# Optimization experiments

Hardware: AMD Instinct MI355X
Metric: run time of the kernel (lower is better)

Reference implementation:

```python
import jax, jax.numpy as jnp
import numpy as np

B, T, D, H = 2, 2048, 1024, 16
STD = 0.02

def setup_inputs() -> dict:
    key = jax.random.key(0)
    ks = jax.random.split(key, 5)
    x = jax.random.normal(ks[0], (B, T, D), dtype=jnp.float32)
    Wq = jax.random.normal(ks[1], (D, D), dtype=jnp.float32) * STD
    Wk = jax.random.normal(ks[2], (D, D), dtype=jnp.float32) * STD
    Wv = jax.random.normal(ks[3], (D, D), dtype=jnp.float32) * STD
    Wo = jax.random.normal(ks[4], (D, D), dtype=jnp.float32) * STD
    z = jnp.zeros((D,), dtype=jnp.float32)
    return {"x": x, "Wq": Wq, "bq": z, "Wk": Wk, "bk": z, "Wv": Wv, "bv": z, "Wo": Wo, "bo": z}

def _split(t, h):
    b, s, dm = t.shape
    return t.reshape(b, s, h, dm // h).transpose(0, 2, 1, 3)  # (B,h,T,d)

def reference(x, Wq, bq, Wk, bk, Wv, bv, Wo, bo):
    h = H
    # linear projections (nn.Linear: y = x @ W^T + b)
    q = _split(x @ Wq.T + bq, h)
    k = _split(x @ Wk.T + bk, h)
    v = _split(x @ Wv.T + bv, h)
    d_k = k.shape[-1]
    # scaled dot-product similarities (B,h,T,T)
    sim = jnp.einsum("bhqd,bhkd->bhqk", q, k) / jnp.sqrt(jnp.float32(d_k))
    # causal mask: upper triangle (excluding diag) filled with -inf
    Tq = sim.shape[-1]
    causal = jnp.tril(jnp.ones((Tq, Tq), dtype=bool))
    sim = jnp.where(causal, sim, -jnp.inf)
    attn = jax.nn.softmax(sim, axis=-1)
    ctx = jnp.einsum("bhqk,bhkd->bhqd", attn, v)  # (B,h,T,d)
    ctx = ctx.transpose(0, 2, 1, 3).reshape(x.shape[0], x.shape[1], -1)  # (B,T,D)
    return ctx @ Wo.T + bo
```

## Files before the change

kernel.cpp:

```cpp
#include <hip/hip_runtime.h>
#include <hip/hip_bf16.h>


typedef __attribute__((ext_vector_type(8))) short bf16x8;
typedef __attribute__((ext_vector_type(4))) float f32x4;
typedef __attribute__((ext_vector_type(4))) short s16x4;

#define QSCALE 0.18033688011f

__device__ __forceinline__ int sniff_f32(const void* p) {
    const unsigned short* u = (const unsigned short*)p;
    int c = 0;
    for (int i = 0; i < 256; ++i) {
        int e = (u[i] >> 7) & 0xFF;
        c += (e >= 0x90) ? 1 : 0;
    }
    return c > 8;
}

__device__ __forceinline__ void async_copy16(const void* g, void* l) {
    __builtin_amdgcn_global_load_lds(
        (const __attribute__((address_space(1))) void*)g,
        (__attribute__((address_space(3))) void*)l, 16, 0, 0);
}

struct Cvt { const void* src; __hip_bfloat16* dst; int n; };
struct CvtPack { Cvt a[9]; };

__global__ __launch_bounds__(256) void cvt_bf16(CvtPack pk) {
    const Cvt c = pk.a[blockIdx.y];
    const int f32 = sniff_f32(c.src);
    const int stride = gridDim.x * 256 * 8;
    for (int idx = (blockIdx.x * 256 + threadIdx.x) * 8; idx < c.n; idx += stride) {
        if (f32) {
            const float* s = (const float*)c.src + idx;
            f32x4 a0 = *(const f32x4*)s;
            f32x4 a1 = *(const f32x4*)(s + 4);
            union { __hip_bfloat16 h[8]; bf16x8 v; } u;
#pragma unroll
            for (int e = 0; e < 4; e++) u.h[e]     = (__hip_bfloat16)a0[e];
#pragma unroll
            for (int e = 0; e < 4; e++) u.h[4 + e] = (__hip_bfloat16)a1[e];
            *(bf16x8*)&c.dst[idx] = u.v;
        } else {
            *(bf16x8*)&c.dst[idx] = *(const bf16x8*)((const __hip_bfloat16*)c.src + idx);
        }
    }
}

template <int MODE>
__device__ __forceinline__ void gemm_async_body(
    const __hip_bfloat16* __restrict__ A, const __hip_bfloat16* __restrict__ W,
    const __hip_bfloat16* __restrict__ bias, void* __restrict__ C,
    int M, int N, int K, int bm, int bn, float outscale,
    __hip_bfloat16* sA, __hip_bfloat16* sB)
{
    const int tid  = threadIdx.x;
    const int wave = tid >> 6;
    const int lane = tid & 63;
    const int quad = lane >> 4;
    const int l15  = lane & 15;
    const int wr   = wave >> 1;
    const int wc   = wave & 1;

    const int srow = wave * 16 + (lane >> 2);
    const int scol = (lane & 3) * 8;
    const __hip_bfloat16* gA0 = A + (size_t)(bm + srow) * K + scol;
    const __hip_bfloat16* gB0 = W + (size_t)(bn + srow) * K + scol;
    __hip_bfloat16* sA0 = sA + wave * 512;
    __hip_bfloat16* sB0 = sB + wave * 512;

    f32x4 acc[4][4];
#pragma unroll
    for (int i = 0; i < 4; i++)
#pragma unroll
        for (int j = 0; j < 4; j++) acc[i][j] = (f32x4)0.0f;

    for (int k0 = 0; k0 < K; k0 += 32) {
        __syncthreads();
#pragma unroll
        for (int r = 0; r < 2; r++) {
            async_copy16(gA0 + (size_t)r * 64 * K + k0, sA0 + r * 2048);
            async_copy16(gB0 + (size_t)r * 64 * K + k0, sB0 + r * 2048);
        }
        __syncthreads();

        bf16x8 af[4], bf[4];
#pragma unroll
        for (int i = 0; i < 4; i++)
            af[i] = *(const bf16x8*)&sA[(wr * 64 + i * 16 + l15) * 32 + quad * 8];
#pragma unroll
        for (int j = 0; j < 4; j++)
            bf[j] = *(const bf16x8*)&sB[(wc * 64 + j * 16 + l15) * 32 + quad * 8];
#pragma unroll
        for (int i = 0; i < 4; i++)
#pragma unroll
            for (int j = 0; j < 4; j++)
                acc[i][j] = __builtin_amdgcn_mfma_f32_16x16x32_bf16(af[i], bf[j], acc[i][j], 0, 0, 0);
    }

    float bv[4];
#pragma unroll
    for (int j = 0; j < 4; j++)
        bv[j] = (float)bias[bn + wc * 64 + j * 16 + l15];

    if (MODE == 2) {
        __hip_bfloat16* VTo = (__hip_bfloat16*)C;
#pragma unroll
        for (int i = 0; i < 4; i++) {
            int tglob = bm + wr * 64 + i * 16 + quad * 4;
            int bb = tglob >> 11, tt = tglob & 2047;
#pragma unroll
            for (int j = 0; j < 4; j++) {
                int d = bn + wc * 64 + j * 16 + l15;
                int hh = d >> 6, dh = d & 63;
                union { __hip_bfloat16 e[4]; s16x4 v; } u;
#pragma unroll
                for (int r = 0; r < 4; r++)
                    u.e[r] = (__hip_bfloat16)(acc[i][j][r] + bv[j]);
                *(s16x4*)&VTo[(((size_t)bb * 16 + hh) * 64 + dh) * 2048 + tt] = u.v;
            }
        }
    } else {
#pragma unroll
        for (int i = 0; i < 4; i++) {
#pragma unroll
            for (int j = 0; j < 4; j++) {
                int col = bn + wc * 64 + j * 16 + l15;
#pragma unroll
                for (int r = 0; r < 4; r++) {
                    int row = bm + wr * 64 + i * 16 + quad * 4 + r;
                    float v = (acc[i][j][r] + bv[j]) * outscale;
                    if (MODE == 1) ((float*)C)[(size_t)row * N + col] = v;
                    else ((__hip_bfloat16*)C)[(size_t)row * N + col] = (__hip_bfloat16)v;
                }
            }
        }
    }
}

__global__ __launch_bounds__(256, 2) void qkv_gemm(
    const __hip_bfloat16* __restrict__ x,
    const __hip_bfloat16* __restrict__ Wq, const __hip_bfloat16* __restrict__ bq, __hip_bfloat16* __restrict__ Q,
    const __hip_bfloat16* __restrict__ Wk, const __hip_bfloat16* __restrict__ bk, __hip_bfloat16* __restrict__ Kb,
    const __hip_bfloat16* __restrict__ Wv, const __hip_bfloat16* __restrict__ bv, __hip_bfloat16* __restrict__ VT,
    int M, int N, int K)
{
    __shared__ __hip_bfloat16 sA[128 * 32];
    __shared__ __hip_bfloat16 sB[128 * 32];
    if (blockIdx.z == 0)
        gemm_async_body<0>(x, Wq, bq, Q, M, N, K, blockIdx.x * 128, blockIdx.y * 128, QSCALE, sA, sB);
    else if (blockIdx.z == 1)
        gemm_async_body<0>(x, Wk, bk, Kb, M, N, K, blockIdx.x * 128, blockIdx.y * 128, 1.0f, sA, sB);
    else
        gemm_async_body<2>(x, Wv, bv, VT, M, N, K, blockIdx.x * 128, blockIdx.y * 128, 1.0f, sA, sB);
}

template <bool OF32>
__device__ __forceinline__ void gemm64_body(
    const __hip_bfloat16* __restrict__ A, const __hip_bfloat16* __restrict__ W,
    const __hip_bfloat16* __restrict__ bias, void* __restrict__ C,
    int M, int N, int K, int bm, int bn,
    __hip_bfloat16* sA, __hip_bfloat16* sB)
{
    const int tid  = threadIdx.x;
    const int wave = tid >> 6;
    const int lane = tid & 63;
    const int quad = lane >> 4;
    const int l15  = lane & 15;

    const int srow = wave * 16 + (lane >> 2);
    const int scol = (lane & 3) * 8;
    const __hip_bfloat16* gA0 = A + (size_t)(bm + srow) * K + scol;
    const __hip_bfloat16* gB0 = W + (size_t)(bn + srow) * K + scol;
    __hip_bfloat16* sA0 = sA + wave * 512;
    __hip_bfloat16* sB0 = sB + wave * 512;

    f32x4 acc[4][2];
#pragma unroll
    for (int i = 0; i < 4; i++)
#pragma unroll
        for (int j = 0; j < 2; j++) acc[i][j] = (f32x4)0.0f;

    for (int k0 = 0; k0 < K; k0 += 32) {
        __syncthreads();
        async_copy16(gA0 + k0, sA0);
#pragma unroll
        for (int r = 0; r < 2; r++)
            async_copy16(gB0 + (size_t)r * 64 * K + k0, sB0 + r * 2048);
        __syncthreads();

        bf16x8 af[4], bf[2];
#pragma unroll
        for (int i = 0; i < 4; i++)
            af[i] = *(const bf16x8*)&sA[(i * 16 + l15) * 32 + quad * 8];
#pragma unroll
        for (int j = 0; j < 2; j++)
            bf[j] = *(const bf16x8*)&sB[(wave * 32 + j * 16 + l15) * 32 + quad * 8];
#pragma unroll
        for (int i = 0; i < 4; i++)
#pragma unroll
            for (int j = 0; j < 2; j++)
                acc[i][j] = __builtin_amdgcn_mfma_f32_16x16x32_bf16(af[i], bf[j], acc[i][j], 0, 0, 0);
    }

    float bv[2];
#pragma unroll
    for (int j = 0; j < 2; j++)
        bv[j] = (float)bias[bn + wave * 32 + j * 16 + l15];
#pragma unroll
    for (int i = 0; i < 4; i++) {
#pragma unroll
        for (int j = 0; j < 2; j++) {
            int col = bn + wave * 32 + j * 16 + l15;
#pragma unroll
            for (int r = 0; r < 4; r++) {
                int row = bm + i * 16 + quad * 4 + r;
                float v = acc[i][j][r] + bv[j];
                if (OF32) ((float*)C)[(size_t)row * N + col] = v;
                else      ((__hip_bfloat16*)C)[(size_t)row * N + col] = (__hip_bfloat16)v;
            }
        }
    }
}

__global__ __launch_bounds__(256, 2) void out_gemm(
    const __hip_bfloat16* __restrict__ A, const __hip_bfloat16* __restrict__ W,
    const __hip_bfloat16* __restrict__ bias, const void* __restrict__ origW,
    void* __restrict__ C, int M, int N, int K)
{
    __shared__ __hip_bfloat16 sA[64 * 32];
    __shared__ __hip_bfloat16 sB[128 * 32];
    __shared__ int f32flag;
    if (threadIdx.x == 0) f32flag = sniff_f32(origW);
    __syncthreads();
    if (f32flag)
        gemm64_body<true>(A, W, bias, C, M, N, K, blockIdx.x * 64, blockIdx.y * 128, sA, sB);
    else
        gemm64_body<false>(A, W, bias, C, M, N, K, blockIdx.x * 64, blockIdx.y * 128, sA, sB);
}

#define PAD 68

__global__ __launch_bounds__(256, 2) void attn_causal(
    const __hip_bfloat16* __restrict__ Q,
    const __hip_bfloat16* __restrict__ K,
    const __hip_bfloat16* __restrict__ VT,
    __hip_bfloat16* __restrict__ O,
    int T, int D, int H)
{
    __shared__ __hip_bfloat16 sK[2][64 * PAD];
    __shared__ __hip_bfloat16 sVT[2][64 * PAD];
    __shared__ __hip_bfloat16 sPA[4][32 * PAD];

    const int tid  = threadIdx.x;
    const int wave = tid >> 6;
    const int lane = tid & 63;
    const int quad = lane >> 4;
    const int l15  = lane & 15;

    const int NT = T >> 7;
    const int qt = blockIdx.z ? (NT - 1 - (int)blockIdx.x) : (int)blockIdx.x;
    const int h  = blockIdx.y;
    const int b  = blockIdx.z;
    const size_t headoff = (size_t)b * T * D + (size_t)h * 64;
    const size_t vtoff   = ((size_t)b * H + h) * 64 * (size_t)T;

    const int nkt = 2 * qt + 2;
    const int myrowmax = qt * 128 + wave * 32 + 31;

    bf16x8 qfrag[2][2];
#pragma unroll
    for (int g = 0; g < 2; g++)
#pragma unroll
        for (int kk = 0; kk < 2; kk++)
            qfrag[g][kk] = *(const bf16x8*)&Q[headoff +
                (size_t)(qt * 128 + wave * 32 + g * 16 + l15) * D + kk * 32 + quad * 8];

    f32x4 acc_o[2][4];
#pragma unroll
    for (int g = 0; g < 2; g++)
#pragma unroll
        for (int j = 0; j < 4; j++) acc_o[g][j] = (f32x4)0.0f;
    float lacc[2] = {0.f, 0.f};

    const int srow = tid >> 3;
    const int sc8  = (tid & 7) * 8;

    bf16x8 pk[2], pv[2];
#pragma unroll
    for (int u = 0; u < 2; u++) {
        int row = srow + u * 32;
        pk[u] = *(const bf16x8*)&K[headoff + (size_t)row * D + sc8];
        pv[u] = *(const bf16x8*)&VT[vtoff + (size_t)row * T + sc8];
    }
#pragma unroll
    for (int u = 0; u < 2; u++) {
        int row = srow + u * 32;
        *(bf16x8*)&sK[0][row * PAD + sc8]  = pk[u];
        *(bf16x8*)&sVT[0][row * PAD + sc8] = pv[u];
    }
    if (nkt > 1) {
#pragma unroll
        for (int u = 0; u < 2; u++) {
            int row = srow + u * 32;
            pk[u] = *(const bf16x8*)&K[headoff + (size_t)(64 + row) * D + sc8];
            pv[u] = *(const bf16x8*)&VT[vtoff + (size_t)row * T + 64 + sc8];
        }
    }
    __syncthreads();

    for (int kt = 0; kt < nkt; ++kt) {
        const int cur = kt & 1;

        if (kt + 1 < nkt) {
#pragma unroll
            for (int u = 0; u < 2; u++) {
                int row = srow + u * 32;
                *(bf16x8*)&sK[1 - cur][row * PAD + sc8]  = pk[u];
                *(bf16x8*)&sVT[1 - cur][row * PAD + sc8] = pv[u];
            }
            if (kt + 2 < nkt) {
#pragma unroll
                for (int u = 0; u < 2; u++) {
                    int row = srow + u * 32;
                    pk[u] = *(const bf16x8*)&K[headoff + (size_t)((kt + 2) * 64 + row) * D + sc8];
                    pv[u] = *(const bf16x8*)&VT[vtoff + (size_t)row * T + (kt + 2) * 64 + sc8];
                }
            }
        }

        if (kt * 64 <= myrowmax) {
            bf16x8 kfrag[2][4], vfrag[2][4];
#pragma unroll
            for (int kk = 0; kk < 2; kk++)
#pragma unroll
                for (int j = 0; j < 4; j++) {
                    kfrag[kk][j] = *(const bf16x8*)&sK[cur][(j * 16 + l15) * PAD + kk * 32 + quad * 8];
                    vfrag[kk][j] = *(const bf16x8*)&sVT[cur][(j * 16 + l15) * PAD + kk * 32 + quad * 8];
                }

#pragma unroll
            for (int g = 0; g < 2; g++) {
                const int qbase = qt * 128 + wave * 32 + g * 16;
                f32x4 st[4];
#pragma unroll
                for (int j = 0; j < 4; j++) st[j] = (f32x4)0.0f;
#pragma unroll
                for (int kk = 0; kk < 2; kk++)
#pragma unroll
                    for (int j = 0; j < 4; j++)
                        st[j] = __builtin_amdgcn_mfma_f32_16x16x32_bf16(
                            kfrag[kk][j], qfrag[g][kk], st[j], 0, 0, 0);

                if (kt * 64 + 63 > qbase) {
                    const int q = qbase + l15;
#pragma unroll
                    for (int j = 0; j < 4; j++) {
                        int keyb = kt * 64 + j * 16 + quad * 4;
#pragma unroll
                        for (int r = 0; r < 4; r++)
                            if (keyb + r > q) st[j][r] = -1e30f;
                    }
                }

#pragma unroll
                for (int j = 0; j < 4; j++) {
                    union { __hip_bfloat16 e[4]; s16x4 v; } u;
#pragma unroll
                    for (int r = 0; r < 4; r++) {
                        float p = exp2f(st[j][r]);
                        lacc[g] += p;
                        u.e[r] = (__hip_bfloat16)p;
                    }
                    *(s16x4*)&sPA[wave][(g * 16 + l15) * PAD + j * 16 + quad * 4] = u.v;
                }
            }
#pragma unroll
            for (int g = 0; g < 2; g++)
#pragma unroll
                for (int kk = 0; kk < 2; kk++) {
                    bf16x8 a = *(const bf16x8*)&sPA[wave][(g * 16 + l15) * PAD + kk * 32 + quad * 8];
#pragma unroll
                    for (int j = 0; j < 4; j++)
                        acc_o[g][j] = __builtin_amdgcn_mfma_f32_16x16x32_bf16(
                            a, vfrag[kk][j], acc_o[g][j], 0, 0, 0);
                }
        }

        __syncthreads();
    }

#pragma unroll
    for (int g = 0; g < 2; g++) {
        lacc[g] += __shfl_xor(lacc[g], 16, 64);
        lacc[g] += __shfl_xor(lacc[g], 32, 64);
    }

#pragma unroll
    for (int g = 0; g < 2; g++)
#pragma unroll
        for (int r = 0; r < 4; r++) {
            float linv = 1.0f / __shfl(lacc[g], quad * 4 + r, 64);
            int row = qt * 128 + wave * 32 + g * 16 + quad * 4 + r;
#pragma unroll
            for (int j = 0; j < 4; j++) {
                int col = j * 16 + l15;
                O[headoff + (size_t)row * D + col] = (__hip_bfloat16)(acc_o[g][j][r] * linv);
            }
        }
}

extern "C" void kernel_launch(void* const* d_in, const int* in_sizes, int n_in,
                              void* d_out, int out_size, void* d_ws, size_t ws_size,
                              hipStream_t stream) {
    const int Bb = 2, T = 2048, D = 1024, H = 16;
    const int M = Bb * T;

    __hip_bfloat16* w = (__hip_bfloat16*)d_ws;
    __hip_bfloat16* Q   = w;
    __hip_bfloat16* Kb  = Q   + (size_t)M * D;
    __hip_bfloat16* VT  = Kb  + (size_t)M * D;
    __hip_bfloat16* ctx = VT  + (size_t)M * D;
    __hip_bfloat16* xb  = ctx + (size_t)M * D;
    __hip_bfloat16* Wqb = xb  + (size_t)M * D;
    __hip_bfloat16* Wkb = Wqb + (size_t)D * D;
    __hip_bfloat16* Wvb = Wkb + (size_t)D * D;
    __hip_bfloat16* Wob = Wvb + (size_t)D * D;
    __hip_bfloat16* bqb = Wob + (size_t)D * D;
    __hip_bfloat16* bkb = bqb + D;
    __hip_bfloat16* bvb = bkb + D;
    __hip_bfloat16* bob = bvb + D;

    CvtPack pk;
    pk.a[0] = { d_in[0], xb,  M * D };
    pk.a[1] = { d_in[1], Wqb, D * D };
    pk.a[2] = { d_in[2], bqb, D };
    pk.a[3] = { d_in[3], Wkb, D * D };
    pk.a[4] = { d_in[4], bkb, D };
    pk.a[5] = { d_in[5], Wvb, D * D };
    pk.a[6] = { d_in[6], bvb, D };
    pk.a[7] = { d_in[7], Wob, D * D };
    pk.a[8] = { d_in[8], bob, D };

    cvt_bf16<<<dim3(512, 9), 256, 0, stream>>>(pk);
    qkv_gemm<<<dim3(M / 128, D / 128, 3), 256, 0, stream>>>(
        xb, Wqb, bqb, Q, Wkb, bkb, Kb, Wvb, bvb, VT, M, D, D);
    attn_causal<<<dim3(T / 128, H, Bb), 256, 0, stream>>>(Q, Kb, VT, ctx, T, D, H);
    out_gemm<<<dim3(M / 64, D / 128), 256, 0, stream>>>(
        ctx, Wob, bob, d_in[7], d_out, M, D, D);
}
```

Measured before the change: 214.8 us.

## Split attention work across 8 waves of 16 query rows each

The causal attention kernel now runs 512 threads per block, so each of 8 waves owns 16 query rows instead of 4 waves owning 32. Each thread stages one K/V row per tile instead of two, which cuts per-thread registers. The change also adds s_setprio around the MFMA sections. It aims to raise occupancy and latency hiding. In exchange, each wave re-reads the K/V fragments from LDS for half as much work, and block barriers now synchronise more waves.

```diff
diff --git a/kernel.cpp b/kernel.cpp
--- a/kernel.cpp
+++ b/kernel.cpp
@@ -242,7 +242,7 @@
 
 #define PAD 68
 
-__global__ __launch_bounds__(256, 2) void attn_causal(
+__global__ __launch_bounds__(512, 4) void attn_causal(
     const __hip_bfloat16* __restrict__ Q,
     const __hip_bfloat16* __restrict__ K,
     const __hip_bfloat16* __restrict__ VT,
@@ -251,7 +251,7 @@
 {
     __shared__ __hip_bfloat16 sK[2][64 * PAD];
     __shared__ __hip_bfloat16 sVT[2][64 * PAD];
-    __shared__ __hip_bfloat16 sPA[4][32 * PAD];
+    __shared__ __hip_bfloat16 sPA[8][16 * PAD];
 
     const int tid  = threadIdx.x;
     const int wave = tid >> 6;
@@ -267,46 +267,31 @@
     const size_t vtoff   = ((size_t)b * H + h) * 64 * (size_t)T;
 
     const int nkt = 2 * qt + 2;
-    const int myrowmax = qt * 128 + wave * 32 + 31;
-
-    bf16x8 qfrag[2][2];
-#pragma unroll
-    for (int g = 0; g < 2; g++)
-#pragma unroll
-        for (int kk = 0; kk < 2; kk++)
-            qfrag[g][kk] = *(const bf16x8*)&Q[headoff +
-                (size_t)(qt * 128 + wave * 32 + g * 16 + l15) * D + kk * 32 + quad * 8];
-
-    f32x4 acc_o[2][4];
-#pragma unroll
-    for (int g = 0; g < 2; g++)
-#pragma unroll
-        for (int j = 0; j < 4; j++) acc_o[g][j] = (f32x4)0.0f;
-    float lacc[2] = {0.f, 0.f};
+    const int qbase    = qt * 128 + wave * 16;
+    const int myrowmax = qbase + 15;
+
+    bf16x8 qfrag[2];
+#pragma unroll
+    for (int kk = 0; kk < 2; kk++)
+        qfrag[kk] = *(const bf16x8*)&Q[headoff +
+            (size_t)(qbase + l15) * D + kk * 32 + quad * 8];
+
+    f32x4 acc_o[4];
+#pragma unroll
+    for (int j = 0; j < 4; j++) acc_o[j] = (f32x4)0.0f;
+    float lacc = 0.f;
 
     const int srow = tid >> 3;
     const int sc8  = (tid & 7) * 8;
 
-    bf16x8 pk[2], pv[2];
-#pragma unroll
-    for (int u = 0; u < 2; u++) {
-        int row = srow + u * 32;
-        pk[u] = *(const bf16x8*)&K[headoff + (size_t)row * D + sc8];
-        pv[u] = *(const bf16x8*)&VT[vtoff + (size_t)row * T + sc8];
-    }
-#pragma unroll
-    for (int u = 0; u < 2; u++) {
-        int row = srow + u * 32;
-        *(bf16x8*)&sK[0][row * PAD + sc8]  = pk[u];
-        *(bf16x8*)&sVT[0][row * PAD + sc8] = pv[u];
-    }
+    bf16x8 pk, pv;
+    pk = *(const bf16x8*)&K[headoff + (size_t)srow * D + sc8];
+    pv = *(const bf16x8*)&VT[vtoff + (size_t)srow * T + sc8];
+    *(bf16x8*)&sK[0][srow * PAD + sc8]  = pk;
+    *(bf16x8*)&sVT[0][srow * PAD + sc8] = pv;
     if (nkt > 1) {
-#pragma unroll
-        for (int u = 0; u < 2; u++) {
-            int row = srow + u * 32;
-            pk[u] = *(const bf16x8*)&K[headoff + (size_t)(64 + row) * D + sc8];
-            pv[u] = *(const bf16x8*)&VT[vtoff + (size_t)row * T + 64 + sc8];
-        }
+        pk = *(const bf16x8*)&K[headoff + (size_t)(64 + srow) * D + sc8];
+        pv = *(const bf16x8*)&VT[vtoff + (size_t)srow * T + 64 + sc8];
     }
     __syncthreads();
 
@@ -314,19 +299,11 @@
         const int cur = kt & 1;
 
         if (kt + 1 < nkt) {
-#pragma unroll
-            for (int u = 0; u < 2; u++) {
-                int row = srow + u * 32;
-                *(bf16x8*)&sK[1 - cur][row * PAD + sc8]  = pk[u];
-                *(bf16x8*)&sVT[1 - cur][row * PAD + sc8] = pv[u];
-            }
+            *(bf16x8*)&sK[1 - cur][srow * PAD + sc8]  = pk;
+            *(bf16x8*)&sVT[1 - cur][srow * PAD + sc8] = pv;
             if (kt + 2 < nkt) {
-#pragma unroll
-                for (int u = 0; u < 2; u++) {
-                    int row = srow + u * 32;
-                    pk[u] = *(const bf16x8*)&K[headoff + (size_t)((kt + 2) * 64 + row) * D + sc8];
-                    pv[u] = *(const bf16x8*)&VT[vtoff + (size_t)row * T + (kt + 2) * 64 + sc8];
-                }
+                pk = *(const bf16x8*)&K[headoff + (size_t)((kt + 2) * 64 + srow) * D + sc8];
+                pv = *(const bf16x8*)&VT[vtoff + (size_t)srow * T + (kt + 2) * 64 + sc8];
             }
         }
 
@@ -340,75 +317,68 @@
                     vfrag[kk][j] = *(const bf16x8*)&sVT[cur][(j * 16 + l15) * PAD + kk * 32 + quad * 8];
                 }
 
-#pragma unroll
-            for (int g = 0; g < 2; g++) {
-                const int qbase = qt * 128 + wave * 32 + g * 16;
-                f32x4 st[4];
-#pragma unroll
-                for (int j = 0; j < 4; j++) st[j] = (f32x4)0.0f;
-#pragma unroll
-                for (int kk = 0; kk < 2; kk++)
-#pragma unroll
-                    for (int j = 0; j < 4; j++)
-                        st[j] = __builtin_amdgcn_mfma_f32_16x16x32_bf16(
-                            kfrag[kk][j], qfrag[g][kk], st[j], 0, 0, 0);
-
-                if (kt * 64 + 63 > qbase) {
-                    const int q = qbase + l15;
-#pragma unroll
-                    for (int j = 0; j < 4; j++) {
-                        int keyb = kt * 64 + j * 16 + quad * 4;
-#pragma unroll
-                        for (int r = 0; r < 4; r++)
-                            if (keyb + r > q) st[j][r] = -1e30f;
-                    }
+            f32x4 st[4];
+#pragma unroll
+            for (int j = 0; j < 4; j++) st[j] = (f32x4)0.0f;
+            __builtin_amdgcn_s_setprio(1);
+#pragma unroll
+            for (int kk = 0; kk < 2; kk++)
+#pragma unroll
+                for (int j = 0; j < 4; j++)
+                    st[j] = __builtin_amdgcn_mfma_f32_16x16x32_bf16(
+                        kfrag[kk][j], qfrag[kk], st[j], 0, 0, 0);
+            __builtin_amdgcn_s_setprio(0);
+
+            if (kt * 64 + 63 > qbase) {
+                const int q = qbase + l15;
+#pragma unroll
+                for (int j = 0; j < 4; j++) {
+                    int keyb = kt * 64 + j * 16 + quad * 4;
+#pragma unroll
+                    for (int r = 0; r < 4; r++)
+                        if (keyb + r > q) st[j][r] = -1e30f;
                 }
-
-#pragma unroll
-                for (int j = 0; j < 4; j++) {
-                    union { __hip_bfloat16 e[4]; s16x4 v; } u;
-#pragma unroll
-                    for (int r = 0; r < 4; r++) {
-                        float p = exp2f(st[j][r]);
-                        lacc[g] += p;
-                        u.e[r] = (__hip_bfloat16)p;
-                    }
-                    *(s16x4*)&sPA[wave][(g * 16 + l15) * PAD + j * 16 + quad * 4] = u.v;
+            }
+
+#pragma unroll
+            for (int j = 0; j < 4; j++) {
+                union { __hip_bfloat16 e[4]; s16x4 v; } u;
+#pragma unroll
+                for (int r = 0; r < 4; r++) {
+                    float p = exp2f(st[j][r]);
+                    lacc += p;
+                    u.e[r] = (__hip_bfloat16)p;
                 }
-            }
-#pragma unroll
-            for (int g = 0; g < 2; g++)
-#pragma unroll
-                for (int kk = 0; kk < 2; kk++) {
-                    bf16x8 a = *(const bf16x8*)&sPA[wave][(g * 16 + l15) * PAD + kk * 32 + quad * 8];
-#pragma unroll
-                    for (int j = 0; j < 4; j++)
-                        acc_o[g][j] = __builtin_amdgcn_mfma_f32_16x16x32_bf16(
-                            a, vfrag[kk][j], acc_o[g][j], 0, 0, 0);
-                }
+                *(s16x4*)&sPA[wave][l15 * PAD + j * 16 + quad * 4] = u.v;
+            }
+            __builtin_amdgcn_s_setprio(1);
+#pragma unroll
+            for (int kk = 0; kk < 2; kk++) {
+                bf16x8 a = *(const bf16x8*)&sPA[wave][l15 * PAD + kk * 32 + quad * 8];
+#pragma unroll
+                for (int j = 0; j < 4; j++)
+                    acc_o[j] = __builtin_amdgcn_mfma_f32_16x16x32_bf16(
+                        a, vfrag[kk][j], acc_o[j], 0, 0, 0);
+            }
+            __builtin_amdgcn_s_setprio(0);
         }
 
         __syncthreads();
     }
 
-#pragma unroll
-    for (int g = 0; g < 2; g++) {
-        lacc[g] += __shfl_xor(lacc[g], 16, 64);
-        lacc[g] += __shfl_xor(lacc[g], 32, 64);
-    }
-
-#pragma unroll
-    for (int g = 0; g < 2; g++)
-#pragma unroll
-        for (int r = 0; r < 4; r++) {
-            float linv = 1.0f / __shfl(lacc[g], quad * 4 + r, 64);
-            int row = qt * 128 + wave * 32 + g * 16 + quad * 4 + r;
-#pragma unroll
-            for (int j = 0; j < 4; j++) {
-                int col = j * 16 + l15;
-                O[headoff + (size_t)row * D + col] = (__hip_bfloat16)(acc_o[g][j][r] * linv);
-            }
-        }
+    lacc += __shfl_xor(lacc, 16, 64);
+    lacc += __shfl_xor(lacc, 32, 64);
+
+#pragma unroll
+    for (int r = 0; r < 4; r++) {
+        float linv = 1.0f / __shfl(lacc, quad * 4 + r, 64);
+        int row = qbase + quad * 4 + r;
+#pragma unroll
+        for (int j = 0; j < 4; j++) {
+            int col = j * 16 + l15;
+            O[headoff + (size_t)row * D + col] = (__hip_bfloat16)(acc_o[j][r] * linv);
+        }
+    }
 }
 
 extern "C" void kernel_launch(void* const* d_in, const int* in_sizes, int n_in,
@@ -446,7 +416,7 @@
     cvt_bf16<<<dim3(512, 9), 256, 0, stream>>>(pk);
     qkv_gemm<<<dim3(M / 128, D / 128, 3), 256, 0, stream>>>(
         xb, Wqb, bqb, Q, Wkb, bkb, Kb, Wvb, bvb, VT, M, D, D);
-    attn_causal<<<dim3(T / 128, H, Bb), 256, 0, stream>>>(Q, Kb, VT, ctx, T, D, H);
+    attn_causal<<<dim3(T / 128, H, Bb), 512, 0, stream>>>(Q, Kb, VT, ctx, T, D, H);
     out_gemm<<<dim3(M / 64, D / 128), 256, 0, stream>>>(
         ctx, Wob, bob, d_in[7], d_out, M, D, D);
 }
```

Result: no change. 211.7 us (-1.4%).

## Split attention key tiles across two wave halves with LDS reduction

Applied to the files above, without the earlier changes.

The attention block grows from 4 to 8 waves. Each query-group wave pair splits every 64-key tile into two 32-key halves, and the pair's partial outputs and row sums are reduced through shared memory at the end. The intent is to double wave-level parallelism per block and cut per-wave register pressure, which gives better latency hiding on the causal workload. s_setprio hints are also added around the MFMA sections. In exchange it adds an epilogue reduction with an extra barrier and gives the half-1 waves idle time on masked tiles.

```diff
diff --git a/kernel.cpp b/kernel.cpp
--- a/kernel.cpp
+++ b/kernel.cpp
@@ -240,24 +240,32 @@
         gemm64_body<false>(A, W, bias, C, M, N, K, blockIdx.x * 64, blockIdx.y * 128, sA, sB);
 }
 
-#define PAD 68
-
-__global__ __launch_bounds__(256, 2) void attn_causal(
+#define PADK 68
+#define PADP 36
+#define KBUF (64 * PADK)
+
+__global__ __launch_bounds__(512, 4) void attn_causal(
     const __hip_bfloat16* __restrict__ Q,
     const __hip_bfloat16* __restrict__ K,
     const __hip_bfloat16* __restrict__ VT,
     __hip_bfloat16* __restrict__ O,
     int T, int D, int H)
 {
-    __shared__ __hip_bfloat16 sK[2][64 * PAD];
-    __shared__ __hip_bfloat16 sVT[2][64 * PAD];
-    __shared__ __hip_bfloat16 sPA[4][32 * PAD];
+    __shared__ __hip_bfloat16 smem[4 * KBUF + 8 * 32 * PADP];
+    __hip_bfloat16* const sKp  = smem;
+    __hip_bfloat16* const sVTp = smem + 2 * KBUF;
 
     const int tid  = threadIdx.x;
     const int wave = tid >> 6;
     const int lane = tid & 63;
     const int quad = lane >> 4;
     const int l15  = lane & 15;
+
+    const int half = wave >> 2;
+    const int qg   = wave & 3;
+    const int koff = half * 32;
+
+    __hip_bfloat16* const sPAw = smem + 4 * KBUF + wave * 32 * PADP;
 
     const int NT = T >> 7;
     const int qt = blockIdx.z ? (NT - 1 - (int)blockIdx.x) : (int)blockIdx.x;
@@ -267,7 +275,8 @@
     const size_t vtoff   = ((size_t)b * H + h) * 64 * (size_t)T;
 
     const int nkt = 2 * qt + 2;
-    const int myrowmax = qt * 128 + wave * 32 + 31;
+    const int qbase    = qt * 128 + qg * 32;
+    const int myrowmax = qbase + 31;
 
     bf16x8 qfrag[2][2];
 #pragma unroll
@@ -275,7 +284,7 @@
 #pragma unroll
         for (int kk = 0; kk < 2; kk++)
             qfrag[g][kk] = *(const bf16x8*)&Q[headoff +
-                (size_t)(qt * 128 + wave * 32 + g * 16 + l15) * D + kk * 32 + quad * 8];
+                (size_t)(qbase + g * 16 + l15) * D + kk * 32 + quad * 8];
 
     f32x4 acc_o[2][4];
 #pragma unroll
@@ -287,77 +296,58 @@
     const int srow = tid >> 3;
     const int sc8  = (tid & 7) * 8;
 
-    bf16x8 pk[2], pv[2];
-#pragma unroll
-    for (int u = 0; u < 2; u++) {
-        int row = srow + u * 32;
-        pk[u] = *(const bf16x8*)&K[headoff + (size_t)row * D + sc8];
-        pv[u] = *(const bf16x8*)&VT[vtoff + (size_t)row * T + sc8];
-    }
-#pragma unroll
-    for (int u = 0; u < 2; u++) {
-        int row = srow + u * 32;
-        *(bf16x8*)&sK[0][row * PAD + sc8]  = pk[u];
-        *(bf16x8*)&sVT[0][row * PAD + sc8] = pv[u];
-    }
+    bf16x8 pk, pv;
+    pk = *(const bf16x8*)&K[headoff + (size_t)srow * D + sc8];
+    pv = *(const bf16x8*)&VT[vtoff + (size_t)srow * T + sc8];
+    *(bf16x8*)&sKp[srow * PADK + sc8]  = pk;
+    *(bf16x8*)&sVTp[srow * PADK + sc8] = pv;
     if (nkt > 1) {
-#pragma unroll
-        for (int u = 0; u < 2; u++) {
-            int row = srow + u * 32;
-            pk[u] = *(const bf16x8*)&K[headoff + (size_t)(64 + row) * D + sc8];
-            pv[u] = *(const bf16x8*)&VT[vtoff + (size_t)row * T + 64 + sc8];
-        }
+        pk = *(const bf16x8*)&K[headoff + (size_t)(64 + srow) * D + sc8];
+        pv = *(const bf16x8*)&VT[vtoff + (size_t)srow * T + 64 + sc8];
     }
     __syncthreads();
 
     for (int kt = 0; kt < nkt; ++kt) {
         const int cur = kt & 1;
+        const __hip_bfloat16* sKc  = sKp  + cur * KBUF;
+        const __hip_bfloat16* sVTc = sVTp + cur * KBUF;
 
         if (kt + 1 < nkt) {
-#pragma unroll
-            for (int u = 0; u < 2; u++) {
-                int row = srow + u * 32;
-                *(bf16x8*)&sK[1 - cur][row * PAD + sc8]  = pk[u];
-                *(bf16x8*)&sVT[1 - cur][row * PAD + sc8] = pv[u];
-            }
+            *(bf16x8*)&sKp[(1 - cur) * KBUF + srow * PADK + sc8]  = pk;
+            *(bf16x8*)&sVTp[(1 - cur) * KBUF + srow * PADK + sc8] = pv;
             if (kt + 2 < nkt) {
-#pragma unroll
-                for (int u = 0; u < 2; u++) {
-                    int row = srow + u * 32;
-                    pk[u] = *(const bf16x8*)&K[headoff + (size_t)((kt + 2) * 64 + row) * D + sc8];
-                    pv[u] = *(const bf16x8*)&VT[vtoff + (size_t)row * T + (kt + 2) * 64 + sc8];
-                }
-            }
-        }
-
-        if (kt * 64 <= myrowmax) {
-            bf16x8 kfrag[2][4], vfrag[2][4];
+                pk = *(const bf16x8*)&K[headoff + (size_t)((kt + 2) * 64 + srow) * D + sc8];
+                pv = *(const bf16x8*)&VT[vtoff + (size_t)srow * T + (kt + 2) * 64 + sc8];
+            }
+        }
+
+        if (kt * 64 + koff <= myrowmax) {
+            bf16x8 kf[2][2];
 #pragma unroll
             for (int kk = 0; kk < 2; kk++)
 #pragma unroll
-                for (int j = 0; j < 4; j++) {
-                    kfrag[kk][j] = *(const bf16x8*)&sK[cur][(j * 16 + l15) * PAD + kk * 32 + quad * 8];
-                    vfrag[kk][j] = *(const bf16x8*)&sVT[cur][(j * 16 + l15) * PAD + kk * 32 + quad * 8];
-                }
+                for (int j = 0; j < 2; j++)
+                    kf[kk][j] = *(const bf16x8*)&sKc[(koff + j * 16 + l15) * PADK + kk * 32 + quad * 8];
 
 #pragma unroll
             for (int g = 0; g < 2; g++) {
-                const int qbase = qt * 128 + wave * 32 + g * 16;
-                f32x4 st[4];
-#pragma unroll
-                for (int j = 0; j < 4; j++) st[j] = (f32x4)0.0f;
+                f32x4 st[2];
+#pragma unroll
+                for (int j = 0; j < 2; j++) st[j] = (f32x4)0.0f;
+                __builtin_amdgcn_s_setprio(1);
 #pragma unroll
                 for (int kk = 0; kk < 2; kk++)
 #pragma unroll
-                    for (int j = 0; j < 4; j++)
+                    for (int j = 0; j < 2; j++)
                         st[j] = __builtin_amdgcn_mfma_f32_16x16x32_bf16(
-                            kfrag[kk][j], qfrag[g][kk], st[j], 0, 0, 0);
-
-                if (kt * 64 + 63 > qbase) {
-                    const int q = qbase + l15;
-#pragma unroll
-                    for (int j = 0; j < 4; j++) {
-                        int keyb = kt * 64 + j * 16 + quad * 4;
+                            kf[kk][j], qfrag[g][kk], st[j], 0, 0, 0);
+                __builtin_amdgcn_s_setprio(0);
+
+                if (kt * 64 + koff + 31 > qbase + g * 16) {
+                    const int q = qbase + g * 16 + l15;
+#pragma unroll
+                    for (int j = 0; j < 2; j++) {
+                        int keyb = kt * 64 + koff + j * 16 + quad * 4;
 #pragma unroll
                         for (int r = 0; r < 4; r++)
                             if (keyb + r > q) st[j][r] = -1e30f;
@@ -365,7 +355,7 @@
                 }
 
 #pragma unroll
-                for (int j = 0; j < 4; j++) {
+                for (int j = 0; j < 2; j++) {
                     union { __hip_bfloat16 e[4]; s16x4 v; } u;
 #pragma unroll
                     for (int r = 0; r < 4; r++) {
@@ -373,19 +363,25 @@
                         lacc[g] += p;
                         u.e[r] = (__hip_bfloat16)p;
                     }
-                    *(s16x4*)&sPA[wave][(g * 16 + l15) * PAD + j * 16 + quad * 4] = u.v;
+                    *(s16x4*)&sPAw[(g * 16 + l15) * PADP + j * 16 + quad * 4] = u.v;
                 }
             }
-#pragma unroll
-            for (int g = 0; g < 2; g++)
-#pragma unroll
-                for (int kk = 0; kk < 2; kk++) {
-                    bf16x8 a = *(const bf16x8*)&sPA[wave][(g * 16 + l15) * PAD + kk * 32 + quad * 8];
-#pragma unroll
-                    for (int j = 0; j < 4; j++)
-                        acc_o[g][j] = __builtin_amdgcn_mfma_f32_16x16x32_bf16(
-                            a, vfrag[kk][j], acc_o[g][j], 0, 0, 0);
-                }
+
+            bf16x8 vf[4];
+#pragma unroll
+            for (int j = 0; j < 4; j++)
+                vf[j] = *(const bf16x8*)&sVTc[(j * 16 + l15) * PADK + koff + quad * 8];
+
+            __builtin_amdgcn_s_setprio(1);
+#pragma unroll
+            for (int g = 0; g < 2; g++) {
+                bf16x8 a = *(const bf16x8*)&sPAw[(g * 16 + l15) * PADP + quad * 8];
+#pragma unroll
+                for (int j = 0; j < 4; j++)
+                    acc_o[g][j] = __builtin_amdgcn_mfma_f32_16x16x32_bf16(
+                        a, vf[j], acc_o[g][j], 0, 0, 0);
+            }
+            __builtin_amdgcn_s_setprio(0);
         }
 
         __syncthreads();
@@ -397,18 +393,43 @@
         lacc[g] += __shfl_xor(lacc[g], 32, 64);
     }
 
-#pragma unroll
-    for (int g = 0; g < 2; g++)
-#pragma unroll
-        for (int r = 0; r < 4; r++) {
-            float linv = 1.0f / __shfl(lacc[g], quad * 4 + r, 64);
-            int row = qt * 128 + wave * 32 + g * 16 + quad * 4 + r;
+    float* const sc  = (float*)smem;
+    float* const lsc = (float*)smem + 8192;
+    if (half == 1) {
+#pragma unroll
+        for (int g = 0; g < 2; g++)
+#pragma unroll
+            for (int j = 0; j < 4; j++)
+                *(f32x4*)&sc[((qg * 8 + g * 4 + j) * 64 + lane) * 4] = acc_o[g][j];
+        if (quad == 0) {
+            lsc[(qg * 2 + 0) * 16 + l15] = lacc[0];
+            lsc[(qg * 2 + 1) * 16 + l15] = lacc[1];
+        }
+    }
+    __syncthreads();
+    if (half == 0) {
+#pragma unroll
+        for (int g = 0; g < 2; g++) {
+            lacc[g] += lsc[(qg * 2 + g) * 16 + l15];
 #pragma unroll
             for (int j = 0; j < 4; j++) {
-                int col = j * 16 + l15;
-                O[headoff + (size_t)row * D + col] = (__hip_bfloat16)(acc_o[g][j][r] * linv);
-            }
-        }
+                f32x4 t = *(const f32x4*)&sc[((qg * 8 + g * 4 + j) * 64 + lane) * 4];
+                acc_o[g][j] += t;
+            }
+        }
+#pragma unroll
+        for (int g = 0; g < 2; g++)
+#pragma unroll
+            for (int r = 0; r < 4; r++) {
+                float linv = 1.0f / __shfl(lacc[g], quad * 4 + r, 64);
+                int row = qbase + g * 16 + quad * 4 + r;
+#pragma unroll
+                for (int j = 0; j < 4; j++) {
+                    int col = j * 16 + l15;
+                    O[headoff + (size_t)row * D + col] = (__hip_bfloat16)(acc_o[g][j][r] * linv);
+                }
+            }
+    }
 }
 
 extern "C" void kernel_launch(void* const* d_in, const int* in_sizes, int n_in,
@@ -446,7 +467,7 @@
     cvt_bf16<<<dim3(512, 9), 256, 0, stream>>>(pk);
     qkv_gemm<<<dim3(M / 128, D / 128, 3), 256, 0, stream>>>(
         xb, Wqb, bqb, Q, Wkb, bkb, Kb, Wvb, bvb, VT, M, D, D);
-    attn_causal<<<dim3(T / 128, H, Bb), 256, 0, stream>>>(Q, Kb, VT, ctx, T, D, H);
+    attn_causal<<<dim3(T / 128, H, Bb), 512, 0, stream>>>(Q, Kb, VT, ctx, T, D, H);
     out_gemm<<<dim3(M / 64, D / 128), 256, 0, stream>>>(
         ctx, Wob, bob, d_in[7], d_out, M, D, D);
 }
```

Result: slower. 256.1 us (+19.2%).
